# Performance work log

Hardware: AMD Instinct MI355X
Metric: run time of the kernel (lower is better)

## Reference

```python
import jax, jax.numpy as jnp
import numpy as np

N = 50000      # nodes
E = 1_600_000  # edges (avg degree 32)
D = 128        # in/hidden channels
OUT = 64       # out channels


def setup_inputs() -> dict:
    key = jax.random.key(0)
    ks = jax.random.split(key, 12)
    s = 0.08  # ~glorot scale for 128-dim
    return {
        "x": jax.random.normal(ks[0], (N, D), jnp.float32),
        "edge_index": jax.random.randint(ks[1], (2, E), 0, N, dtype=jnp.int64),
        # GCN layer 1
        "W1": jax.random.normal(ks[2], (D, D), jnp.float32) * s,
        "b1": jnp.zeros((D,), jnp.float32),
        # GraphSAGE layer 2 (mean aggregation): lin_l on neighbors, lin_r on root
        "Wl": jax.random.normal(ks[3], (D, D), jnp.float32) * s,
        "Wr": jax.random.normal(ks[4], (D, D), jnp.float32) * s,
        "bs": jnp.zeros((D,), jnp.float32),
        # GAT layer 3 (heads=1, concat=False)
        "Wg": jax.random.normal(ks[5], (D, D), jnp.float32) * s,
        "a_s": jax.random.normal(ks[6], (D,), jnp.float32) * s,
        "a_d": jax.random.normal(ks[7], (D,), jnp.float32) * s,
        "bg": jnp.zeros((D,), jnp.float32),
        # GCN output layer
        "Wo": jax.random.normal(ks[8], (D, OUT), jnp.float32) * s,
        "bo": jnp.zeros((OUT,), jnp.float32),
    }


def _self_loops(src, dst, n):
    loop = jnp.arange(n, dtype=src.dtype)
    return jnp.concatenate([src, loop]), jnp.concatenate([dst, loop])


def gcn_conv(x, W, b, src, dst, n):
    # PyG GCNConv: add self-loops, symmetric normalization D^-1/2 (A+I) D^-1/2
    s2, d2 = _self_loops(src, dst, n)
    deg = jax.ops.segment_sum(jnp.ones_like(d2, dtype=x.dtype), d2, num_segments=n)
    dinv = jnp.where(deg > 0, jax.lax.rsqrt(deg), 0.0)
    h = x @ W                         # [n, out]
    norm = dinv[s2] * dinv[d2]        # [E+n]
    out = jax.ops.segment_sum(h[s2] * norm[:, None], d2, num_segments=n)
    return out + b


def sage_conv(x, Wl, Wr, b, src, dst, n):
    # PyG SAGEConv, aggr='mean': W_l * mean_neigh + W_r * x (no self-loops)
    deg = jax.ops.segment_sum(jnp.ones_like(dst, dtype=x.dtype), dst, num_segments=n)
    agg = jax.ops.segment_sum(x[src], dst, num_segments=n)
    mean = agg / jnp.maximum(deg, 1.0)[:, None]
    return mean @ Wl + x @ Wr + b


def gat_conv(x, W, a_s, a_d, b, src, dst, n):
    # PyG GATConv heads=1, concat=False: self-loops, edge softmax over incoming edges
    h = x @ W                               # [n, out]
    s2, d2 = _self_loops(src, dst, n)
    alpha_src = h @ a_s                     # [n]
    alpha_dst = h @ a_d                     # [n]
    e = jax.nn.leaky_relu(alpha_src[s2] + alpha_dst[d2], negative_slope=0.2)
    m = jax.ops.segment_max(e, d2, num_segments=n)   # every node has a self-loop
    ex = jnp.exp(e - m[d2])
    denom = jax.ops.segment_sum(ex, d2, num_segments=n)
    alpha = ex / denom[d2]
    out = jax.ops.segment_sum(alpha[:, None] * h[s2], d2, num_segments=n)
    return out + b


def reference(x, edge_index, W1, b1, Wl, Wr, bs, Wg, a_s, a_d, bg, Wo, bo):
    src, dst = edge_index[0], edge_index[1]
    n = x.shape[0]
    # eval mode: F.dropout(training=False) is identity
    h = jax.nn.relu(gcn_conv(x, W1, b1, src, dst, n))
    h = jax.nn.relu(sage_conv(h, Wl, Wr, bs, src, dst, n))
    h = jax.nn.relu(gat_conv(h, Wg, a_s, a_d, bg, src, dst, n))
    return gcn_conv(h, Wo, bo, src, dst, n)
```

## Files before the change

kernel.cpp:

```cpp
#include <hip/hip_runtime.h>
#include <math.h>


#define BUCKET_BITS 8
#define BUCKET_SZ   256
#define NBMAX       256
#define CAP         10240
#define CAPE        2560

typedef short short8 __attribute__((ext_vector_type(8)));
typedef float f32x4 __attribute__((ext_vector_type(4)));
typedef float f32x2 __attribute__((ext_vector_type(2)));
typedef unsigned int u32x4 __attribute__((ext_vector_type(4)));
typedef unsigned short u16x8 __attribute__((ext_vector_type(8)));

__device__ __forceinline__ float leaky02(float x) { return x > 0.0f ? x : 0.2f * x; }
__device__ __forceinline__ float bflo(unsigned u) { return __uint_as_float(u << 16); }
__device__ __forceinline__ float bfhi(unsigned u) { return __uint_as_float(u & 0xFFFF0000u); }
__device__ __forceinline__ unsigned short f2bf(float f) {
    unsigned u = __float_as_uint(f);
    u += 0x7FFFu + ((u >> 16) & 1u);
    return (unsigned short)(u >> 16);
}

__global__ __launch_bounds__(256) void wpackall_k(
    const float* __restrict__ W1, const float* __restrict__ Wl,
    const float* __restrict__ Wr, const float* __restrict__ Wg,
    const float* __restrict__ Wo,
    unsigned* __restrict__ P1, unsigned* __restrict__ Pl,
    unsigned* __restrict__ Pr, unsigned* __restrict__ Pg,
    unsigned* __restrict__ Po)
{
    const int b = blockIdx.x;
    const float* W; unsigned* P; int NO;
    if      (b == 0) { W = W1; P = P1; NO = 128; }
    else if (b == 1) { W = Wl; P = Pl; NO = 128; }
    else if (b == 2) { W = Wr; P = Pr; NO = 128; }
    else if (b == 3) { W = Wg; P = Pg; NO = 128; }
    else             { W = Wo; P = Po; NO = 64;  }
    const int CT = NO / 16;
    const int n4w = NO / 4;
    for (int f = threadIdx.x; f < 64 * n4w; f += 256) {
        const int kp = f / n4w;
        const int n4 = f % n4w;
        const float4 a = *(const float4*)(W + (size_t)(2 * kp) * NO + n4 * 4);
        const float4 bb = *(const float4*)(W + (size_t)(2 * kp + 1) * NO + n4 * 4);
        const int k = 2 * kp, kb = k >> 5, qq = (k >> 3) & 3, p = (k & 7) >> 1;
        const float av[4] = {a.x, a.y, a.z, a.w};
        const float bv[4] = {bb.x, bb.y, bb.z, bb.w};
#pragma unroll
        for (int j = 0; j < 4; j++) {
            int col = n4 * 4 + j;
            int c = col >> 4, nl = col & 15;
            unsigned pk = (unsigned)f2bf(av[j]) | ((unsigned)f2bf(bv[j]) << 16);
            P[(((kb * CT + c) * 64) + qq * 16 + nl) * 4 + p] = pk;
        }
    }
}

template<int NO, bool AFP32, bool SCALE, bool BIASRELU, bool DUAL, bool DOTS>
__global__ __launch_bounds__(256) void mgemm_k(
    const void* __restrict__ Av, const unsigned short* __restrict__ Bp,
    const void* __restrict__ A1v, const unsigned short* __restrict__ Bp1,
    unsigned short* __restrict__ C16,
    const float* __restrict__ scale, const float* __restrict__ bias,
    const float* __restrict__ a_s, const float* __restrict__ a_d,
    float* __restrict__ as_, float* __restrict__ ad_, int n)
{
    constexpr int CT = NO / 16;
    const int tid = threadIdx.x;
    const int wave = tid >> 6, lane = tid & 63;
    const int q = lane >> 4, ml = lane & 15;
    const int row0 = blockIdx.x * 64 + wave * 16;
    int arow = row0 + ml; if (arow >= n) arow = n - 1;

    f32x4 acc[CT];
#pragma unroll
    for (int c = 0; c < CT; c++) acc[c] = {0.f, 0.f, 0.f, 0.f};

    for (int half = 0; half < (DUAL ? 2 : 1); half++) {
        const unsigned short* __restrict__ Bsrc = half ? Bp1 : Bp;
        const void* Asrc = half ? A1v : Av;
#pragma unroll
        for (int kb = 0; kb < 4; kb++) {
            short8 afr;
            if (AFP32) {
                const float* Af = (const float*)Asrc + (size_t)arow * 128 + kb * 32 + q * 8;
                float4 f0 = *(const float4*)Af;
                float4 f1 = *(const float4*)(Af + 4);
                afr[0] = (short)f2bf(f0.x); afr[1] = (short)f2bf(f0.y);
                afr[2] = (short)f2bf(f0.z); afr[3] = (short)f2bf(f0.w);
                afr[4] = (short)f2bf(f1.x); afr[5] = (short)f2bf(f1.y);
                afr[6] = (short)f2bf(f1.z); afr[7] = (short)f2bf(f1.w);
            } else {
                afr = *(const short8*)((const unsigned short*)Asrc +
                                       ((size_t)kb * n + arow) * 32 + q * 8);
            }
            short8 bfr[CT];
#pragma unroll
            for (int c = 0; c < CT; c++)
                bfr[c] = *(const short8*)(Bsrc + ((size_t)(kb * CT + c) * 64 + lane) * 8);
#pragma unroll
            for (int c = 0; c < CT; c++)
                acc[c] = __builtin_amdgcn_mfma_f32_16x16x32_bf16(afr, bfr[c], acc[c], 0, 0, 0);
        }
    }

    if (DOTS) {
        float ps[4] = {0.f, 0.f, 0.f, 0.f}, pd[4] = {0.f, 0.f, 0.f, 0.f};
#pragma unroll
        for (int c = 0; c < CT; c++) {
            float sv = a_s[c * 16 + ml], dv = a_d[c * 16 + ml];
#pragma unroll
            for (int r = 0; r < 4; r++) {
                ps[r] = fmaf(acc[c][r], sv, ps[r]);
                pd[r] = fmaf(acc[c][r], dv, pd[r]);
            }
        }
#pragma unroll
        for (int off = 1; off < 16; off <<= 1) {
#pragma unroll
            for (int r = 0; r < 4; r++) {
                ps[r] += __shfl_xor(ps[r], off, 64);
                pd[r] += __shfl_xor(pd[r], off, 64);
            }
        }
        if (ml == 0) {
#pragma unroll
            for (int r = 0; r < 4; r++) {
                int row = row0 + q * 4 + r;
                if (row < n) { as_[row] = ps[r]; ad_[row] = pd[r]; }
            }
        }
    }

    float sc[4];
    if (SCALE) {
#pragma unroll
        for (int r = 0; r < 4; r++) {
            int row = row0 + q * 4 + r;
            sc[r] = scale[row < n ? row : 0];
        }
    }
#pragma unroll
    for (int c = 0; c < CT; c++) {
        float bv = BIASRELU ? bias[c * 16 + ml] : 0.0f;
        const int col = c * 16 + ml;
#pragma unroll
        for (int r = 0; r < 4; r++) {
            int row = row0 + q * 4 + r;
            if (row < n) {
                float v = acc[c][r];
                if (SCALE) v *= sc[r];
                if (BIASRELU) v = fmaxf(v + bv, 0.0f);
                C16[((size_t)(col >> 5) * n + row) * 32 + (col & 31)] = f2bf(v);
            }
        }
    }
}

__global__ void binit_k(int* __restrict__ bcur, int nb) {
    int t = threadIdx.x;
    if (t < nb) bcur[t] = t * CAP;
}

#define PART_CH 4096
__global__ __launch_bounds__(256) void part_k(
    const int* __restrict__ src, const int* __restrict__ dst,
    int* __restrict__ bcur, unsigned long long* __restrict__ part, int nE)
{
    __shared__ int cnt[NBMAX];
    __shared__ int cur[NBMAX];
    const int base = blockIdx.x * PART_CH;
    const int t = threadIdx.x;
    cnt[t] = 0;
    __syncthreads();
    int d[PART_CH / 256], s[PART_CH / 256];
#pragma unroll
    for (int j = 0; j < PART_CH / 256; j++) {
        int e = base + j * 256 + t;
        if (e < nE) {
            d[j] = dst[e]; s[j] = src[e];
            atomicAdd(&cnt[d[j] >> BUCKET_BITS], 1);
        } else d[j] = -1;
    }
    __syncthreads();
    {
        int c = cnt[t];
        cur[t] = c ? atomicAdd(&bcur[t], c) : 0;
    }
    __syncthreads();
#pragma unroll
    for (int j = 0; j < PART_CH / 256; j++) {
        if (d[j] >= 0) {
            int p = atomicAdd(&cur[d[j] >> BUCKET_BITS], 1);
            part[p] = ((unsigned long long)(unsigned)d[j] << 32) | (unsigned)s[j];
        }
    }
}

__global__ __launch_bounds__(256) void bscan_k(const int* __restrict__ bcur,
                                               int* __restrict__ bofs, int nb) {
    __shared__ int sm[256];
    const int t = threadIdx.x;
    int v = (t < nb) ? (bcur[t] - t * CAP) : 0;
    sm[t] = v;
    __syncthreads();
    for (int off = 1; off < 256; off <<= 1) {
        int tv = (t >= off) ? sm[t - off] : 0;
        __syncthreads();
        sm[t] += tv;
        __syncthreads();
    }
    if (t < nb) {
        bofs[t] = sm[t] - v;
        if (t == nb - 1) bofs[nb] = sm[t];
    }
}

__global__ __launch_bounds__(256) void csr_k(
    const unsigned long long* __restrict__ part, const int* __restrict__ bcur,
    const int* __restrict__ bofs, int* __restrict__ rowptr, int* __restrict__ srcs,
    float* __restrict__ dinv, float* __restrict__ invm, int n, int nE)
{
    __shared__ int lcnt[BUCKET_SZ];
    __shared__ int sm[BUCKET_SZ];
    __shared__ int lcur[BUCKET_SZ];
    const int b = blockIdx.x;
    const int t = threadIdx.x;
    const int base_in = b * CAP;
    const int cntE = bcur[b] - base_in;
    const int base_out = bofs[b];

    lcnt[t] = 0;
    __syncthreads();
#pragma unroll 4
    for (int e = t; e < cntE; e += 256) {
        int dl = (int)(part[base_in + e] >> 32) & (BUCKET_SZ - 1);
        atomicAdd(&lcnt[dl], 1);
    }
    __syncthreads();
    int v = lcnt[t];
    sm[t] = v;
    __syncthreads();
    for (int off = 1; off < 256; off <<= 1) {
        int tv = (t >= off) ? sm[t - off] : 0;
        __syncthreads();
        sm[t] += tv;
        __syncthreads();
    }
    const int excl = sm[t] - v;
    const int node = (b << BUCKET_BITS) + t;
    if (node < n) {
        rowptr[node] = base_out + excl;
        float dg = (float)v;
        dinv[node] = rsqrtf(dg + 1.0f);
        invm[node] = 1.0f / fmaxf(dg, 1.0f);
        if (node == n - 1) rowptr[n] = nE;
    }
    lcur[t] = excl;
    __syncthreads();
#pragma unroll 4
    for (int e = t; e < cntE; e += 256) {
        unsigned long long w = part[base_in + e];
        int dl = (int)(w >> 32) & (BUCKET_SZ - 1);
        int pos = atomicAdd(&lcur[dl], 1);
        srcs[base_out + pos] = (int)(unsigned)w;
    }
}

__global__ __launch_bounds__(256) void gatw_k(
    const int* __restrict__ rowptr, const int* __restrict__ srcs,
    const float* __restrict__ as_, const float* __restrict__ ad_,
    float* __restrict__ ew, float* __restrict__ rdn_, float* __restrict__ sw_, int n)
{
    const int node = blockIdx.x * 32 + (threadIdx.x >> 3);
    const int lane = threadIdx.x & 7;
    if (node >= n) return;
    const int beg = rowptr[node], end = rowptr[node + 1];
    const float ad_d = ad_[node];
    float psum = 0.f;
    for (int k = beg + lane; k < end; k += 8) {
        float e = __expf(leaky02(as_[srcs[k]] + ad_d));
        ew[k] = e;
        psum += e;
    }
#pragma unroll
    for (int off = 4; off > 0; off >>= 1) psum += __shfl_xor(psum, off, 64);
    if (lane == 0) {
        float se = __expf(leaky02(as_[node] + ad_d));
        float r = 1.0f / (psum + se);
        rdn_[node] = r;
        sw_[node] = se * r;
    }
}

template<int MODE, bool OV>
__device__ __forceinline__ void gath_loop(
    const char* __restrict__ Hb, unsigned loff,
    const int* __restrict__ srcs, const float* __restrict__ ew,
    const int* lsrc, const float* lw,
    int beg, int end, int beg_blk, f32x2* acc)
{
    int k = beg;
    for (; k + 8 <= end; k += 8) {
        int s[8]; float wv[8];
#pragma unroll
        for (int j = 0; j < 8; j++) {
            int ofs = k + j - beg_blk;
            if (OV) {
                bool in = ofs < CAPE;
                int ofc = in ? ofs : 0;
                s[j] = in ? lsrc[ofc] : srcs[k + j];
                if (MODE == 2) wv[j] = in ? lw[ofc] : ew[k + j];
            } else {
                s[j] = lsrc[ofs];
                if (MODE == 2) wv[j] = lw[ofs];
            }
        }
        u32x4 h[8];
#pragma unroll
        for (int j = 0; j < 8; j++)
            h[j] = *(const u32x4*)(Hb + (size_t)(((unsigned)s[j] << 6) + loff));
#pragma unroll
        for (int j = 0; j < 8; j++) {
            f32x2 w2 = {wv[j], wv[j]};
#pragma unroll
            for (int c = 0; c < 4; c++) {
                f32x2 hv = {bflo(h[j][c]), bfhi(h[j][c])};
                if (MODE == 2) acc[c] = w2 * hv + acc[c];
                else           acc[c] = acc[c] + hv;
            }
        }
    }
    if (k < end) {
        int s[8]; float wv[8];
#pragma unroll
        for (int j = 0; j < 8; j++) {
            int kk = k + j;
            bool act = kk < end;
            int kc = act ? kk : end - 1;
            int ofs = kc - beg_blk;
            int sj; float w0 = 1.0f;
            if (OV) {
                bool in = ofs < CAPE;
                int ofc = in ? ofs : 0;
                sj = in ? lsrc[ofc] : srcs[kc];
                if (MODE == 2) w0 = in ? lw[ofc] : ew[kc];
            } else {
                sj = lsrc[ofs];
                if (MODE == 2) w0 = lw[ofs];
            }
            s[j] = sj;
            wv[j] = act ? ((MODE == 2) ? w0 : 1.0f) : 0.0f;
        }
        u32x4 h[8];
#pragma unroll
        for (int j = 0; j < 8; j++)
            h[j] = *(const u32x4*)(Hb + (size_t)(((unsigned)s[j] << 6) + loff));
#pragma unroll
        for (int j = 0; j < 8; j++) {
            f32x2 w2 = {wv[j], wv[j]};
#pragma unroll
            for (int c = 0; c < 4; c++) {
                f32x2 hv = {bflo(h[j][c]), bfhi(h[j][c])};
                acc[c] = w2 * hv + acc[c];
            }
        }
    }
}

template<int NCB, int MODE>
__global__ __launch_bounds__(256) void gatherbf_k(
    const unsigned short* __restrict__ H16, float* __restrict__ outf,
    unsigned short* __restrict__ out16,
    const int* __restrict__ rowptr, const int* __restrict__ srcs,
    const float* __restrict__ scl,
    const float* __restrict__ sw_,
    const float* __restrict__ ew,
    const float* __restrict__ bias, int n)
{
    constexpr int XPC = 8 / NCB;
    constexpr int NPB = 64;
    __shared__ int lsrc[CAPE];
    __shared__ float lw[(MODE == 2) ? CAPE : 1];

    const int bid = (int)blockIdx.x;
    const int xj = bid & 7;
    const int cb = xj / XPC;
    const int NG = (n + NPB - 1) / NPB;
    const int ng = (bid >> 3) * XPC + (xj % XPC);
    if (ng >= NG) return;

    const int tid = (int)threadIdx.x;
    const int node0 = ng * NPB;
    const int nodeN = min(node0 + NPB, n);
    const int beg_blk = rowptr[node0];
    const int end_blk = rowptr[nodeN];
    const int cnt = end_blk - beg_blk;
    const int cl = min(cnt, CAPE);
    for (int i = tid; i < cl; i += 256) {
        lsrc[i] = srcs[beg_blk + i];
        if (MODE == 2) lw[i] = ew[beg_blk + i];
    }
    __syncthreads();

    const int node = node0 + (tid >> 2);
    const int lane = tid & 3;
    if (node >= nodeN) return;
    const int beg = rowptr[node], end = rowptr[node + 1];
    const char* __restrict__ Hb = (const char*)H16 + (size_t)cb * n * 64;
    const unsigned loff = (unsigned)lane * 16u;

    f32x2 acc[4];
#pragma unroll
    for (int c = 0; c < 4; c++) acc[c] = {0.f, 0.f};

    if (cnt <= CAPE)
        gath_loop<MODE, false>(Hb, loff, srcs, ew, lsrc, lw, beg, end, beg_blk, acc);
    else
        gath_loop<MODE, true>(Hb, loff, srcs, ew, lsrc, lw, beg, end, beg_blk, acc);

    const size_t orow = ((size_t)cb * n + node) * 4 + lane;
    float r[8];
    if (MODE == 0) {
        float sc = scl[node];
#pragma unroll
        for (int c = 0; c < 4; c++) { r[2*c] = acc[c].x * sc; r[2*c+1] = acc[c].y * sc; }
    } else {
        u32x4 su = *(const u32x4*)(Hb + (size_t)(((unsigned)node << 6) + loff));
        float sv[8];
#pragma unroll
        for (int c = 0; c < 4; c++) { sv[2*c] = bflo(su[c]); sv[2*c+1] = bfhi(su[c]); }
        const float4* b4 = (const float4*)bias;
        float4 ba = b4[cb * 8 + lane * 2], bb = b4[cb * 8 + lane * 2 + 1];
        float bv[8] = {ba.x, ba.y, ba.z, ba.w, bb.x, bb.y, bb.z, bb.w};
        float a8[8];
#pragma unroll
        for (int c = 0; c < 4; c++) { a8[2*c] = acc[c].x; a8[2*c+1] = acc[c].y; }
        if (MODE == 2) {
            float rden = scl[node], sw = sw_[node];
#pragma unroll
            for (int j = 0; j < 8; j++)
                r[j] = fmaxf(fmaf(rden, a8[j], fmaf(sw, sv[j], bv[j])), 0.f);
        } else {
            float dv = scl[node];
#pragma unroll
            for (int j = 0; j < 8; j++) {
                r[j] = dv * (a8[j] + sv[j]) + bv[j];
                if (MODE == 1) r[j] = fmaxf(r[j], 0.f);
            }
        }
    }
    if (MODE == 3) {
        float4* o4 = (float4*)(outf + (size_t)node * 64 + cb * 32 + lane * 8);
        float4 ra = {r[0], r[1], r[2], r[3]}, rb = {r[4], r[5], r[6], r[7]};
        o4[0] = ra; o4[1] = rb;
    } else {
        u16x8 qv;
#pragma unroll
        for (int j = 0; j < 8; j++) qv[j] = f2bf(r[j]);
        ((u16x8*)out16)[orow] = qv;
    }
}

extern "C" void kernel_launch(void* const* d_in, const int* in_sizes, int n_in,
                              void* d_out, int out_size, void* d_ws, size_t ws_size,
                              hipStream_t stream)
{
    const float* x   = (const float*)d_in[0];
    const int*   ei  = (const int*)d_in[1];
    const float* W1  = (const float*)d_in[2];
    const float* b1  = (const float*)d_in[3];
    const float* Wl  = (const float*)d_in[4];
    const float* Wr  = (const float*)d_in[5];
    const float* bs  = (const float*)d_in[6];
    const float* Wg  = (const float*)d_in[7];
    const float* a_s = (const float*)d_in[8];
    const float* a_d = (const float*)d_in[9];
    const float* bg  = (const float*)d_in[10];
    const float* Wo  = (const float*)d_in[11];
    const float* bo  = (const float*)d_in[12];

    const int n  = in_sizes[0] / 128;
    const int nE = in_sizes[1] / 2;
    const int* src = ei;
    const int* dst = ei + nE;

    char* w = (char*)d_ws;
    auto alloc = [&](size_t bytes) { char* p = w; w += (bytes + 255) & ~(size_t)255; return p; };
    unsigned short* S0 = (unsigned short*)alloc((size_t)n * 128 * 2);
    unsigned short* S1 = (unsigned short*)alloc((size_t)n * 128 * 2);
    unsigned short* S2 = (unsigned short*)alloc((size_t)n * 128 * 2);
    const int nbv = (n + BUCKET_SZ - 1) / BUCKET_SZ;
    unsigned long long* part = (unsigned long long*)alloc((size_t)nbv * CAP * 8);
    int*   srcs   = (int*)alloc((size_t)nE * 4);
    float* ew     = (float*)alloc((size_t)nE * 4);
    int*   rowptr = (int*)alloc((size_t)(n + 1) * 4);
    int*   bofs   = (int*)alloc((NBMAX + 1) * 4);
    int*   bcur   = (int*)alloc(NBMAX * 4);
    float* dinv   = (float*)alloc((size_t)n * 4);
    float* invm   = (float*)alloc((size_t)n * 4);
    float* as_    = (float*)alloc((size_t)n * 4);
    float* ad_    = (float*)alloc((size_t)n * 4);
    float* rdn_   = (float*)alloc((size_t)n * 4);
    float* sw_    = (float*)alloc((size_t)n * 4);
    unsigned* P1  = (unsigned*)alloc(64 * 128 * 4);
    unsigned* Pl  = (unsigned*)alloc(64 * 128 * 4);
    unsigned* Pr  = (unsigned*)alloc(64 * 128 * 4);
    unsigned* Pg  = (unsigned*)alloc(64 * 128 * 4);
    unsigned* Po  = (unsigned*)alloc(64 * 64 * 4);

    const int TB = 256;
    auto cdiv = [](long long a, long long b) { return (int)((a + b - 1) / b); };
    const int nb     = nbv;
    const int gPart  = cdiv(nE, PART_CH);
    const int gGemm  = cdiv(n, 64);
    const int NG     = cdiv(n, 64);
    const int gGa128 = 8 * cdiv(NG, 2);
    const int gGa64  = 8 * cdiv(NG, 4);
    const int gGatw  = cdiv(n, 32);

    wpackall_k<<<5, TB, 0, stream>>>(W1, Wl, Wr, Wg, Wo, P1, Pl, Pr, Pg, Po);
    binit_k<<<1, 256, 0, stream>>>(bcur, nb);
    part_k<<<gPart, TB, 0, stream>>>(src, dst, bcur, part, nE);
    bscan_k<<<1, 256, 0, stream>>>(bcur, bofs, nb);
    csr_k<<<nb, TB, 0, stream>>>(part, bcur, bofs, rowptr, srcs, dinv, invm, n, nE);

    mgemm_k<128, true, true, false, false, false><<<gGemm, TB, 0, stream>>>(
        x, (const unsigned short*)P1, nullptr, nullptr, S0, dinv, nullptr,
        nullptr, nullptr, nullptr, nullptr, n);
    gatherbf_k<4, 1><<<gGa128, TB, 0, stream>>>(S0, nullptr, S1, rowptr, srcs,
                                                dinv, nullptr, nullptr, b1, n);

    gatherbf_k<4, 0><<<gGa128, TB, 0, stream>>>(S1, nullptr, S0, rowptr, srcs,
                                                invm, nullptr, nullptr, nullptr, n);
    mgemm_k<128, false, false, true, true, false><<<gGemm, TB, 0, stream>>>(
        S0, (const unsigned short*)Pl, S1, (const unsigned short*)Pr, S2,
        nullptr, bs, nullptr, nullptr, nullptr, nullptr, n);

    mgemm_k<128, false, false, false, false, true><<<gGemm, TB, 0, stream>>>(
        S2, (const unsigned short*)Pg, nullptr, nullptr, S1, nullptr, nullptr,
        a_s, a_d, as_, ad_, n);
    gatw_k<<<gGatw, TB, 0, stream>>>(rowptr, srcs, as_, ad_, ew, rdn_, sw_, n);
    gatherbf_k<4, 2><<<gGa128, TB, 0, stream>>>(S1, nullptr, S0, rowptr, srcs,
                                                rdn_, sw_, ew, bg, n);

    mgemm_k<64, false, true, false, false, false><<<gGemm, TB, 0, stream>>>(
        S0, (const unsigned short*)Po, nullptr, nullptr, S2, dinv, nullptr,
        nullptr, nullptr, nullptr, nullptr, n);
    gatherbf_k<2, 3><<<gGa64, TB, 0, stream>>>(S2, (float*)d_out, nullptr, rowptr, srcs,
                                               dinv, nullptr, nullptr, bo, n);
}
```

Measured before the change: 351.2 us.

## Shrink gather blocks, unroll gather by 16, fuse scan and init launches

Merges the bucket-counter init into the weight-packing kernel and moves the bucket prefix scan into each csr_k block, which removes two tiny kernel launches. The gather kernels now run 128-thread blocks covering 32 nodes each, with half the shared-memory edge cache, to raise occupancy. A 16-wide unrolled gather loop is added to put more loads in flight. The costs are a redundant scan in every csr_k block, more register pressure from the wider unroll, and more edges spilling past the smaller cache to global reads.

```diff
diff --git a/kernel.cpp b/kernel.cpp
--- a/kernel.cpp
+++ b/kernel.cpp
@@ -6,7 +6,7 @@
 #define BUCKET_SZ   256
 #define NBMAX       256
 #define CAP         10240
-#define CAPE        2560
+#define CAPE        1280
 
 typedef short short8 __attribute__((ext_vector_type(8)));
 typedef float f32x4 __attribute__((ext_vector_type(4)));
@@ -29,9 +29,14 @@
     const float* __restrict__ Wo,
     unsigned* __restrict__ P1, unsigned* __restrict__ Pl,
     unsigned* __restrict__ Pr, unsigned* __restrict__ Pg,
-    unsigned* __restrict__ Po)
+    unsigned* __restrict__ Po, int* __restrict__ bcur, int nb)
 {
     const int b = blockIdx.x;
+    if (b == 5) {
+        int t = threadIdx.x;
+        if (t < nb) bcur[t] = t * CAP;
+        return;
+    }
     const float* W; unsigned* P; int NO;
     if      (b == 0) { W = W1; P = P1; NO = 128; }
     else if (b == 1) { W = Wl; P = Pl; NO = 128; }
@@ -159,11 +164,6 @@
     }
 }
 
-__global__ void binit_k(int* __restrict__ bcur, int nb) {
-    int t = threadIdx.x;
-    if (t < nb) bcur[t] = t * CAP;
-}
-
 #define PART_CH 4096
 __global__ __launch_bounds__(256) void part_k(
     const int* __restrict__ src, const int* __restrict__ dst,
@@ -199,29 +199,10 @@
     }
 }
 
-__global__ __launch_bounds__(256) void bscan_k(const int* __restrict__ bcur,
-                                               int* __restrict__ bofs, int nb) {
-    __shared__ int sm[256];
-    const int t = threadIdx.x;
-    int v = (t < nb) ? (bcur[t] - t * CAP) : 0;
-    sm[t] = v;
-    __syncthreads();
-    for (int off = 1; off < 256; off <<= 1) {
-        int tv = (t >= off) ? sm[t - off] : 0;
-        __syncthreads();
-        sm[t] += tv;
-        __syncthreads();
-    }
-    if (t < nb) {
-        bofs[t] = sm[t] - v;
-        if (t == nb - 1) bofs[nb] = sm[t];
-    }
-}
-
 __global__ __launch_bounds__(256) void csr_k(
     const unsigned long long* __restrict__ part, const int* __restrict__ bcur,
-    const int* __restrict__ bofs, int* __restrict__ rowptr, int* __restrict__ srcs,
-    float* __restrict__ dinv, float* __restrict__ invm, int n, int nE)
+    int* __restrict__ rowptr, int* __restrict__ srcs,
+    float* __restrict__ dinv, float* __restrict__ invm, int n, int nE, int nb)
 {
     __shared__ int lcnt[BUCKET_SZ];
     __shared__ int sm[BUCKET_SZ];
@@ -230,7 +211,18 @@
     const int t = threadIdx.x;
     const int base_in = b * CAP;
     const int cntE = bcur[b] - base_in;
-    const int base_out = bofs[b];
+
+    int vb = (t < nb) ? (bcur[t] - t * CAP) : 0;
+    sm[t] = vb;
+    __syncthreads();
+    for (int off = 1; off < 256; off <<= 1) {
+        int tv = (t >= off) ? sm[t - off] : 0;
+        __syncthreads();
+        sm[t] += tv;
+        __syncthreads();
+    }
+    const int base_out = sm[b] - (bcur[b] - b * CAP);
+    __syncthreads();
 
     lcnt[t] = 0;
     __syncthreads();
@@ -303,6 +295,36 @@
     int beg, int end, int beg_blk, f32x2* acc)
 {
     int k = beg;
+    for (; k + 16 <= end; k += 16) {
+        int s[16]; float wv[16];
+#pragma unroll
+        for (int j = 0; j < 16; j++) {
+            int ofs = k + j - beg_blk;
+            if (OV) {
+                bool in = ofs < CAPE;
+                int ofc = in ? ofs : 0;
+                s[j] = in ? lsrc[ofc] : srcs[k + j];
+                if (MODE == 2) wv[j] = in ? lw[ofc] : ew[k + j];
+            } else {
+                s[j] = lsrc[ofs];
+                if (MODE == 2) wv[j] = lw[ofs];
+            }
+        }
+        u32x4 h[16];
+#pragma unroll
+        for (int j = 0; j < 16; j++)
+            h[j] = *(const u32x4*)(Hb + (size_t)(((unsigned)s[j] << 6) + loff));
+#pragma unroll
+        for (int j = 0; j < 16; j++) {
+            f32x2 w2 = {wv[j], wv[j]};
+#pragma unroll
+            for (int c = 0; c < 4; c++) {
+                f32x2 hv = {bflo(h[j][c]), bfhi(h[j][c])};
+                if (MODE == 2) acc[c] = w2 * hv + acc[c];
+                else           acc[c] = acc[c] + hv;
+            }
+        }
+    }
     for (; k + 8 <= end; k += 8) {
         int s[8]; float wv[8];
 #pragma unroll
@@ -371,7 +393,7 @@
 }
 
 template<int NCB, int MODE>
-__global__ __launch_bounds__(256) void gatherbf_k(
+__global__ __launch_bounds__(128, 4) void gatherbf_k(
     const unsigned short* __restrict__ H16, float* __restrict__ outf,
     unsigned short* __restrict__ out16,
     const int* __restrict__ rowptr, const int* __restrict__ srcs,
@@ -381,7 +403,7 @@
     const float* __restrict__ bias, int n)
 {
     constexpr int XPC = 8 / NCB;
-    constexpr int NPB = 64;
+    constexpr int NPB = 32;
     __shared__ int lsrc[CAPE];
     __shared__ float lw[(MODE == 2) ? CAPE : 1];
 
@@ -399,7 +421,7 @@
     const int end_blk = rowptr[nodeN];
     const int cnt = end_blk - beg_blk;
     const int cl = min(cnt, CAPE);
-    for (int i = tid; i < cl; i += 256) {
+    for (int i = tid; i < cl; i += 128) {
         lsrc[i] = srcs[beg_blk + i];
         if (MODE == 2) lw[i] = ew[beg_blk + i];
     }
@@ -497,7 +519,6 @@
     int*   srcs   = (int*)alloc((size_t)nE * 4);
     float* ew     = (float*)alloc((size_t)nE * 4);
     int*   rowptr = (int*)alloc((size_t)(n + 1) * 4);
-    int*   bofs   = (int*)alloc((NBMAX + 1) * 4);
     int*   bcur   = (int*)alloc(NBMAX * 4);
     float* dinv   = (float*)alloc((size_t)n * 4);
     float* invm   = (float*)alloc((size_t)n * 4);
@@ -516,25 +537,23 @@
     const int nb     = nbv;
     const int gPart  = cdiv(nE, PART_CH);
     const int gGemm  = cdiv(n, 64);
-    const int NG     = cdiv(n, 64);
+    const int NG     = cdiv(n, 32);
     const int gGa128 = 8 * cdiv(NG, 2);
     const int gGa64  = 8 * cdiv(NG, 4);
     const int gGatw  = cdiv(n, 32);
 
-    wpackall_k<<<5, TB, 0, stream>>>(W1, Wl, Wr, Wg, Wo, P1, Pl, Pr, Pg, Po);
-    binit_k<<<1, 256, 0, stream>>>(bcur, nb);
+    wpackall_k<<<6, TB, 0, stream>>>(W1, Wl, Wr, Wg, Wo, P1, Pl, Pr, Pg, Po, bcur, nb);
     part_k<<<gPart, TB, 0, stream>>>(src, dst, bcur, part, nE);
-    bscan_k<<<1, 256, 0, stream>>>(bcur, bofs, nb);
-    csr_k<<<nb, TB, 0, stream>>>(part, bcur, bofs, rowptr, srcs, dinv, invm, n, nE);
+    csr_k<<<nb, TB, 0, stream>>>(part, bcur, rowptr, srcs, dinv, invm, n, nE, nb);
 
     mgemm_k<128, true, true, false, false, false><<<gGemm, TB, 0, stream>>>(
         x, (const unsigned short*)P1, nullptr, nullptr, S0, dinv, nullptr,
         nullptr, nullptr, nullptr, nullptr, n);
-    gatherbf_k<4, 1><<<gGa128, TB, 0, stream>>>(S0, nullptr, S1, rowptr, srcs,
-                                                dinv, nullptr, nullptr, b1, n);
-
-    gatherbf_k<4, 0><<<gGa128, TB, 0, stream>>>(S1, nullptr, S0, rowptr, srcs,
-                                                invm, nullptr, nullptr, nullptr, n);
+    gatherbf_k<4, 1><<<gGa128, 128, 0, stream>>>(S0, nullptr, S1, rowptr, srcs,
+                                                 dinv, nullptr, nullptr, b1, n);
+
+    gatherbf_k<4, 0><<<gGa128, 128, 0, stream>>>(S1, nullptr, S0, rowptr, srcs,
+                                                 invm, nullptr, nullptr, nullptr, n);
     mgemm_k<128, false, false, true, true, false><<<gGemm, TB, 0, stream>>>(
         S0, (const unsigned short*)Pl, S1, (const unsigned short*)Pr, S2,
         nullptr, bs, nullptr, nullptr, nullptr, nullptr, n);
@@ -543,12 +562,12 @@
         S2, (const unsigned short*)Pg, nullptr, nullptr, S1, nullptr, nullptr,
         a_s, a_d, as_, ad_, n);
     gatw_k<<<gGatw, TB, 0, stream>>>(rowptr, srcs, as_, ad_, ew, rdn_, sw_, n);
-    gatherbf_k<4, 2><<<gGa128, TB, 0, stream>>>(S1, nullptr, S0, rowptr, srcs,
-                                                rdn_, sw_, ew, bg, n);
+    gatherbf_k<4, 2><<<gGa128, 128, 0, stream>>>(S1, nullptr, S0, rowptr, srcs,
+                                                 rdn_, sw_, ew, bg, n);
 
     mgemm_k<64, false, true, false, false, false><<<gGemm, TB, 0, stream>>>(
         S0, (const unsigned short*)Po, nullptr, nullptr, S2, dinv, nullptr,
         nullptr, nullptr, nullptr, nullptr, n);
-    gatherbf_k<2, 3><<<gGa64, TB, 0, stream>>>(S2, (float*)d_out, nullptr, rowptr, srcs,
-                                               dinv, nullptr, nullptr, bo, n);
-}
+    gatherbf_k<2, 3><<<gGa64, 128, 0, stream>>>(S2, (float*)d_out, nullptr, rowptr, srcs,
+                                                dinv, nullptr, nullptr, bo, n);
+}
```

Result: faster. 343.5 us (-2.2%).
